# Optimization experiments

Hardware: AMD Instinct MI355X
Metric: run time of the kernel (lower is better)

The kernel has to match this reference:

```python
import jax, jax.numpy as jnp
import numpy as np


def setup_inputs() -> dict:
    key = jax.random.key(0)
    k1, k2, k3 = jax.random.split(key, 3)
    B, P, E, H = 256, 512, 256, 128
    x = jax.random.normal(k1, (B, P, E), dtype=jnp.float32)
    # torch Linear weights are [out, in]; init uniform(-0.1, 0.1)
    w1 = jax.random.uniform(k2, (H, E), minval=-0.1, maxval=0.1, dtype=jnp.float32)
    w2 = jax.random.uniform(k3, (1, H), minval=-0.1, maxval=0.1, dtype=jnp.float32)
    return {"x": x, "w1": w1, "w2": w2}


def reference(x, w1, w2):
    # scores: [B, P] = tanh(x @ w1.T) @ w2.T
    h = jnp.tanh(jnp.einsum('bpe,he->bph', x, w1))
    scores = jnp.einsum('bph,h->bp', h, w2[0])
    weight = jax.nn.softmax(scores, axis=1)            # softmax over pool dim
    pooled = jnp.einsum('bp,bpe->be', weight, x)       # weighted-sum pool
    return pooled
```

## Files before the change

### kernel.cpp

```cpp
#include <hip/hip_runtime.h>

#define NB 256
#define NP 512
#define NE 256
#define NH 128
#define PT 64
#define HALF 256
#define NT (HALF / PT)
#define RS 264

typedef __attribute__((ext_vector_type(8))) short bf16x8;
typedef __attribute__((ext_vector_type(4))) short short4v;
typedef __attribute__((ext_vector_type(4))) float f32x4;

__device__ __forceinline__ short f2bf(float f) {
  union { float f; unsigned u; } v; v.f = f;
  unsigned r = v.u + 0x7fffu + ((v.u >> 16) & 1u);
  return (short)(r >> 16);
}
__device__ __forceinline__ float bf2f(short s) {
  union { unsigned u; float f; } v;
  v.u = ((unsigned)(unsigned short)s) << 16;
  return v.f;
}
__device__ __forceinline__ float fast_tanh(float x) {
  float u = __builtin_amdgcn_exp2f(x * 2.8853900817779268f);
  return 1.0f - 2.0f * __builtin_amdgcn_rcpf(u + 1.0f);
}

__global__ __launch_bounds__(512, 4) void pathattn_part(
    const float* __restrict__ x, const float* __restrict__ w1,
    const float* __restrict__ w2, float* __restrict__ wsPool,
    float* __restrict__ wsZ) {
  __shared__ short xs[2][PT * RS];
  __shared__ float sp[8][PT];
  __shared__ float expw[PT];
  __shared__ float pool2[2][NE];

  const int tid  = threadIdx.x;
  const int lane = tid & 63;
  const int wid  = tid >> 6;
  const int b    = blockIdx.x >> 1;
  const int half = blockIdx.x & 1;
  const float* xb = x + (size_t)b * NP * NE + (size_t)half * HALF * NE;

  bf16x8 bfrag[8];
  float w2v;
  const int n15 = lane & 15;
  const int kg8 = (lane >> 4) * 8;
  {
    const int j = wid * 16 + n15;
    w2v = w2[j];
    #pragma unroll
    for (int kt = 0; kt < 8; ++kt) {
      const f32x4* s = (const f32x4*)(w1 + j * NE + kt * 32 + kg8);
      f32x4 a = s[0], c = s[1];
      bf16x8 v;
      v[0]=f2bf(a[0]); v[1]=f2bf(a[1]); v[2]=f2bf(a[2]); v[3]=f2bf(a[3]);
      v[4]=f2bf(c[0]); v[5]=f2bf(c[1]); v[6]=f2bf(c[2]); v[7]=f2bf(c[3]);
      bfrag[kt] = v;
    }
  }

  f32x4 streg[8];
  auto issue_loads = [&](int tile) {
    const float* base = xb + tile * PT * NE;
    #pragma unroll
    for (int rr = 0; rr < 8; ++rr) {
      int f   = rr * 512 + tid;
      int row = f >> 6;
      int c4  = f & 63;
      streg[rr] = *(const f32x4*)(base + row * NE + c4 * 4);
    }
  };
  auto write_tile = [&](int buf) {
    #pragma unroll
    for (int rr = 0; rr < 8; ++rr) {
      int f   = rr * 512 + tid;
      int row = f >> 6;
      int c4  = f & 63;
      short4v v;
      v[0]=f2bf(streg[rr][0]); v[1]=f2bf(streg[rr][1]);
      v[2]=f2bf(streg[rr][2]); v[3]=f2bf(streg[rr][3]);
      *(short4v*)(&xs[buf][row * RS + c4 * 4]) = v;
    }
  };

  issue_loads(0);
  write_tile(0);
  __syncthreads();

  float pacc = 0.f;
  float zacc = 0.f;
  const int pe = tid & 255;
  const int pq = tid >> 8;

  for (int t = 0; t < NT; ++t) {
    const int cur = t & 1;
    if (t + 1 < NT) issue_loads(t + 1);

    f32x4 acc[4];
    #pragma unroll
    for (int rt = 0; rt < 4; ++rt) acc[rt] = (f32x4){0.f,0.f,0.f,0.f};
    #pragma unroll
    for (int kt = 0; kt < 8; ++kt) {
      #pragma unroll
      for (int rt = 0; rt < 4; ++rt) {
        bf16x8 av = *(const bf16x8*)(&xs[cur][(rt*16 + n15) * RS + kt*32 + kg8]);
        acc[rt] = __builtin_amdgcn_mfma_f32_16x16x32_bf16(av, bfrag[kt], acc[rt], 0, 0, 0);
      }
    }
    float sc[4][4];
    #pragma unroll
    for (int rt = 0; rt < 4; ++rt)
      #pragma unroll
      for (int r = 0; r < 4; ++r)
        sc[rt][r] = fast_tanh(acc[rt][r]) * w2v;
    #pragma unroll
    for (int m = 1; m <= 8; m <<= 1)
      #pragma unroll
      for (int rt = 0; rt < 4; ++rt)
        #pragma unroll
        for (int r = 0; r < 4; ++r)
          sc[rt][r] += __shfl_xor(sc[rt][r], m, 64);
    if (n15 == 0) {
      #pragma unroll
      for (int rt = 0; rt < 4; ++rt) {
        const int rbase = rt * 16 + (lane >> 4) * 4;
        #pragma unroll
        for (int r = 0; r < 4; ++r) sp[wid][rbase + r] = sc[rt][r];
      }
    }
    __syncthreads();

    if (tid < PT) {
      float s = 0.f;
      #pragma unroll
      for (int w = 0; w < 8; ++w) s += sp[w][tid];
      float e = __builtin_amdgcn_exp2f(s * 1.4426950408889634f);
      expw[tid] = e;
      zacc += e;
    }
    __syncthreads();

    #pragma unroll
    for (int pp = 0; pp < 32; ++pp) {
      const int p = pq * 32 + pp;
      pacc += expw[p] * bf2f(xs[cur][p * RS + pe]);
    }

    if (t + 1 < NT) {
      write_tile(cur ^ 1);
      __syncthreads();
    }
  }

  pool2[pq][pe] = pacc;
  float z = zacc;
  if (wid == 0) {
    #pragma unroll
    for (int m = 1; m <= 32; m <<= 1) z += __shfl_xor(z, m, 64);
  }
  __syncthreads();
  if (tid < NE)
    wsPool[(size_t)blockIdx.x * NE + tid] = pool2[0][tid] + pool2[1][tid];
  if (tid == 0)
    wsZ[blockIdx.x] = z;
}

__global__ void pathattn_combine(const float* __restrict__ wsPool,
                                 const float* __restrict__ wsZ,
                                 float* __restrict__ out) {
  const int b = blockIdx.x, e = threadIdx.x;
  float v = wsPool[(size_t)(2*b) * NE + e] + wsPool[(size_t)(2*b+1) * NE + e];
  float z = wsZ[2*b] + wsZ[2*b+1];
  out[(size_t)b * NE + e] = v / z;
}

extern "C" void kernel_launch(void* const* d_in, const int* in_sizes, int n_in,
                              void* d_out, int out_size, void* d_ws, size_t ws_size,
                              hipStream_t stream) {
  (void)in_sizes; (void)n_in; (void)out_size; (void)ws_size;
  const float* x  = (const float*)d_in[0];
  const float* w1 = (const float*)d_in[1];
  const float* w2 = (const float*)d_in[2];
  float* out = (float*)d_out;
  float* wsPool = (float*)d_ws;
  float* wsZ    = wsPool + 512 * NE;
  pathattn_part<<<2 * NB, 512, 0, stream>>>(x, w1, w2, wsPool, wsZ);
  pathattn_combine<<<NB, NE, 0, stream>>>(wsPool, wsZ, out);
}
```

Before: 45.84 us.

## Swap MFMA operands to cut score shuffles, drop a barrier, vectorize pooling

The MFMA operands are swapped so that W1 is the A operand and x rows are the B operand. Each lane's accumulator then holds four H values for a single pool row, which replaces the 4-step xor-shuffle reduction with an in-register sum plus two shuffles. Every wave now recomputes the exp weights redundantly and distributes them by shuffle, which removes the expw shared array and one __syncthreads per tile. The weighted-sum pool reads 8 bf16 values per LDS access into 16 partial row-group accumulators, reduced at the end through shared memory unioned with the tile buffers. The cost is more exp work per wave and a larger final reduction.

```diff
diff --git a/kernel.cpp b/kernel.cpp
--- a/kernel.cpp
+++ b/kernel.cpp
@@ -8,6 +8,7 @@
 #define HALF 256
 #define NT (HALF / PT)
 #define RS 264
+#define SP_LD 68
 
 typedef __attribute__((ext_vector_type(8))) short bf16x8;
 typedef __attribute__((ext_vector_type(4))) short short4v;
@@ -28,38 +29,45 @@
   return 1.0f - 2.0f * __builtin_amdgcn_rcpf(u + 1.0f);
 }
 
+union SMem {
+  struct {
+    short xs[2][PT * RS];
+    float sp[8][SP_LD];
+  } s;
+  float pool[16][NE];
+};
+
 __global__ __launch_bounds__(512, 4) void pathattn_part(
     const float* __restrict__ x, const float* __restrict__ w1,
     const float* __restrict__ w2, float* __restrict__ wsPool,
     float* __restrict__ wsZ) {
-  __shared__ short xs[2][PT * RS];
-  __shared__ float sp[8][PT];
-  __shared__ float expw[PT];
-  __shared__ float pool2[2][NE];
+  __shared__ SMem sm;
 
   const int tid  = threadIdx.x;
   const int lane = tid & 63;
   const int wid  = tid >> 6;
+  const int n15  = lane & 15;
+  const int l4   = lane >> 4;
+  const int kg8  = l4 * 8;
   const int b    = blockIdx.x >> 1;
   const int half = blockIdx.x & 1;
   const float* xb = x + (size_t)b * NP * NE + (size_t)half * HALF * NE;
 
-  bf16x8 bfrag[8];
-  float w2v;
-  const int n15 = lane & 15;
-  const int kg8 = (lane >> 4) * 8;
+  bf16x8 afrag[8];
+  float w2v[4];
   {
-    const int j = wid * 16 + n15;
-    w2v = w2[j];
+    const int h = wid * 16 + n15;
     #pragma unroll
     for (int kt = 0; kt < 8; ++kt) {
-      const f32x4* s = (const f32x4*)(w1 + j * NE + kt * 32 + kg8);
+      const f32x4* s = (const f32x4*)(w1 + h * NE + kt * 32 + kg8);
       f32x4 a = s[0], c = s[1];
       bf16x8 v;
       v[0]=f2bf(a[0]); v[1]=f2bf(a[1]); v[2]=f2bf(a[2]); v[3]=f2bf(a[3]);
       v[4]=f2bf(c[0]); v[5]=f2bf(c[1]); v[6]=f2bf(c[2]); v[7]=f2bf(c[3]);
-      bfrag[kt] = v;
+      afrag[kt] = v;
     }
+    #pragma unroll
+    for (int r = 0; r < 4; ++r) w2v[r] = w2[wid * 16 + l4 * 4 + r];
   }
 
   f32x4 streg[8];
@@ -82,7 +90,7 @@
       short4v v;
       v[0]=f2bf(streg[rr][0]); v[1]=f2bf(streg[rr][1]);
       v[2]=f2bf(streg[rr][2]); v[3]=f2bf(streg[rr][3]);
-      *(short4v*)(&xs[buf][row * RS + c4 * 4]) = v;
+      *(short4v*)(&sm.s.xs[buf][row * RS + c4 * 4]) = v;
     }
   };
 
@@ -90,82 +98,79 @@
   write_tile(0);
   __syncthreads();
 
-  float pacc = 0.f;
+  const int rowg  = tid >> 5;
+  const int chunk = tid & 31;
+  f32x4 pacc0 = {0.f,0.f,0.f,0.f}, pacc1 = {0.f,0.f,0.f,0.f};
   float zacc = 0.f;
-  const int pe = tid & 255;
-  const int pq = tid >> 8;
 
   for (int t = 0; t < NT; ++t) {
     const int cur = t & 1;
     if (t + 1 < NT) issue_loads(t + 1);
 
+    const short* xcur = sm.s.xs[cur];
     f32x4 acc[4];
     #pragma unroll
-    for (int rt = 0; rt < 4; ++rt) acc[rt] = (f32x4){0.f,0.f,0.f,0.f};
+    for (int pt = 0; pt < 4; ++pt) acc[pt] = (f32x4){0.f,0.f,0.f,0.f};
     #pragma unroll
     for (int kt = 0; kt < 8; ++kt) {
       #pragma unroll
-      for (int rt = 0; rt < 4; ++rt) {
-        bf16x8 av = *(const bf16x8*)(&xs[cur][(rt*16 + n15) * RS + kt*32 + kg8]);
-        acc[rt] = __builtin_amdgcn_mfma_f32_16x16x32_bf16(av, bfrag[kt], acc[rt], 0, 0, 0);
+      for (int pt = 0; pt < 4; ++pt) {
+        bf16x8 bv = *(const bf16x8*)(&xcur[(pt * 16 + n15) * RS + kt * 32 + kg8]);
+        acc[pt] = __builtin_amdgcn_mfma_f32_16x16x32_bf16(afrag[kt], bv, acc[pt], 0, 0, 0);
       }
     }
-    float sc[4][4];
     #pragma unroll
-    for (int rt = 0; rt < 4; ++rt)
+    for (int pt = 0; pt < 4; ++pt) {
+      float s = 0.f;
       #pragma unroll
-      for (int r = 0; r < 4; ++r)
-        sc[rt][r] = fast_tanh(acc[rt][r]) * w2v;
-    #pragma unroll
-    for (int m = 1; m <= 8; m <<= 1)
-      #pragma unroll
-      for (int rt = 0; rt < 4; ++rt)
-        #pragma unroll
-        for (int r = 0; r < 4; ++r)
-          sc[rt][r] += __shfl_xor(sc[rt][r], m, 64);
-    if (n15 == 0) {
-      #pragma unroll
-      for (int rt = 0; rt < 4; ++rt) {
-        const int rbase = rt * 16 + (lane >> 4) * 4;
-        #pragma unroll
-        for (int r = 0; r < 4; ++r) sp[wid][rbase + r] = sc[rt][r];
-      }
+      for (int r = 0; r < 4; ++r) s += fast_tanh(acc[pt][r]) * w2v[r];
+      s += __shfl_xor(s, 16, 64);
+      s += __shfl_xor(s, 32, 64);
+      if (l4 == 0) sm.s.sp[wid][pt * 16 + n15] = s;
     }
     __syncthreads();
 
-    if (tid < PT) {
-      float s = 0.f;
-      #pragma unroll
-      for (int w = 0; w < 8; ++w) s += sp[w][tid];
-      float e = __builtin_amdgcn_exp2f(s * 1.4426950408889634f);
-      expw[tid] = e;
-      zacc += e;
-    }
-    __syncthreads();
+    float ssum = 0.f;
+    #pragma unroll
+    for (int w = 0; w < 8; ++w) ssum += sm.s.sp[w][lane];
+    float e = __builtin_amdgcn_exp2f(ssum * 1.4426950408889634f);
+    zacc += e;
 
     #pragma unroll
-    for (int pp = 0; pp < 32; ++pp) {
-      const int p = pq * 32 + pp;
-      pacc += expw[p] * bf2f(xs[cur][p * RS + pe]);
+    for (int it = 0; it < 4; ++it) {
+      const int p   = rowg * 4 + it;
+      const int src = wid * 8 + (lane >> 5) * 4 + it;
+      float ep = __shfl(e, src, 64);
+      bf16x8 v = *(const bf16x8*)(&xcur[p * RS + chunk * 8]);
+      pacc0[0] += ep * bf2f(v[0]);
+      pacc0[1] += ep * bf2f(v[1]);
+      pacc0[2] += ep * bf2f(v[2]);
+      pacc0[3] += ep * bf2f(v[3]);
+      pacc1[0] += ep * bf2f(v[4]);
+      pacc1[1] += ep * bf2f(v[5]);
+      pacc1[2] += ep * bf2f(v[6]);
+      pacc1[3] += ep * bf2f(v[7]);
     }
 
-    if (t + 1 < NT) {
-      write_tile(cur ^ 1);
-      __syncthreads();
-    }
+    if (t + 1 < NT) write_tile(cur ^ 1);
+    __syncthreads();
   }
 
-  pool2[pq][pe] = pacc;
-  float z = zacc;
+  *(f32x4*)(&sm.pool[rowg][chunk * 8])     = pacc0;
+  *(f32x4*)(&sm.pool[rowg][chunk * 8 + 4]) = pacc1;
+  __syncthreads();
+  if (tid < NE) {
+    float v = 0.f;
+    #pragma unroll
+    for (int rg = 0; rg < 16; ++rg) v += sm.pool[rg][tid];
+    wsPool[(size_t)blockIdx.x * NE + tid] = v;
+  }
   if (wid == 0) {
+    float z = zacc;
     #pragma unroll
     for (int m = 1; m <= 32; m <<= 1) z += __shfl_xor(z, m, 64);
+    if (lane == 0) wsZ[blockIdx.x] = z;
   }
-  __syncthreads();
-  if (tid < NE)
-    wsPool[(size_t)blockIdx.x * NE + tid] = pool2[0][tid] + pool2[1][tid];
-  if (tid == 0)
-    wsZ[blockIdx.x] = z;
 }
 
 __global__ void pathattn_combine(const float* __restrict__ wsPool,
```

Result: faster. 39.11 us (-14.7%).
